# Kernel tuning notes

Hardware: AMD Instinct MI355X
Metric: run time of the kernel (lower is better)

Reference implementation:

```python
import jax, jax.numpy as jnp
import numpy as np

D_MODEL = 1024
NUM_HEADS = 16
D_K = D_MODEL // NUM_HEADS  # 64
THETA = 10000.0


def apply_rope(t, positions):
    # t: [b, h, s, d], positions: [s] int
    d = t.shape[-1]
    inv_freq = 1.0 / (THETA ** (jnp.arange(0, d, 2, dtype=jnp.float32) / d))  # [d/2]
    ang = positions.astype(jnp.float32)[:, None] * inv_freq[None, :]  # [s, d/2]
    cos = jnp.cos(ang)[None, None]  # [1,1,s,d/2]
    sin = jnp.sin(ang)[None, None]
    x1 = t[..., 0::2]
    x2 = t[..., 1::2]
    r1 = x1 * cos - x2 * sin
    r2 = x1 * sin + x2 * cos
    # interleave back: [..., d/2, 2] -> [..., d]
    return jnp.stack([r1, r2], axis=-1).reshape(t.shape)


def setup_inputs() -> dict:
    key = jax.random.key(0)
    ks = jax.random.split(key, 5)
    b, s = 4, 2048
    scale = 1.0 / np.sqrt(D_MODEL)
    return {
        "x": jax.random.normal(ks[0], (b, s, D_MODEL), dtype=jnp.float32),
        "Wq": jax.random.normal(ks[1], (D_MODEL, D_MODEL), dtype=jnp.float32) * scale,
        "Wk": jax.random.normal(ks[2], (D_MODEL, D_MODEL), dtype=jnp.float32) * scale,
        "Wv": jax.random.normal(ks[3], (D_MODEL, D_MODEL), dtype=jnp.float32) * scale,
        "Wo": jax.random.normal(ks[4], (D_MODEL, D_MODEL), dtype=jnp.float32) * scale,
        "token_positions": jnp.arange(s, dtype=jnp.int32),
    }


def reference(x, Wq, Wk, Wv, Wo, token_positions):
    b, s, _ = x.shape
    # nn.Linear with no bias: y = x @ W.T
    def proj(W):
        y = jnp.einsum('bsd,ed->bse', x, W)
        return y.reshape(b, s, NUM_HEADS, D_K).transpose(0, 2, 1, 3)  # [b,h,s,dk]
    Q = apply_rope(proj(Wq), token_positions)
    K = apply_rope(proj(Wk), token_positions)
    V = proj(Wv)
    scores = jnp.einsum('bhqd,bhkd->bhqk', Q, K) / np.sqrt(D_K).astype(np.float32)
    causal = jnp.arange(s)[:, None] >= jnp.arange(s)[None, :]  # [s,s] lower-tri True
    scores = jnp.where(causal[None, None], scores, -jnp.inf)
    probs = jax.nn.softmax(scores, axis=-1)
    out = jnp.einsum('bhqk,bhkd->bhqd', probs, V)  # [b,h,s,dk]
    out = out.transpose(0, 2, 1, 3).reshape(b, s, D_MODEL)
    return jnp.einsum('bsd,ed->bse', out, Wo)
```

## Files before the change

### kernel.cpp

```cpp
#include <hip/hip_runtime.h>
#include <stdint.h>

#define SLEN 2048
#define DMODEL 1024
#define NHEADS 16
#define MTOT 8192

typedef short s16x8 __attribute__((ext_vector_type(8)));
typedef short s16x4 __attribute__((ext_vector_type(4)));
typedef float f32x4 __attribute__((ext_vector_type(4)));
typedef float f32x16 __attribute__((ext_vector_type(16)));
typedef unsigned u32x2 __attribute__((ext_vector_type(2)));
typedef unsigned u32x4 __attribute__((ext_vector_type(4)));

static __device__ __forceinline__ unsigned short f2bf(float f) {
  unsigned u = __builtin_bit_cast(unsigned, f);
  u += 0x7fffu + ((u >> 16) & 1u);
  return (unsigned short)(u >> 16);
}

static __device__ __forceinline__ unsigned cvt_pk_bf16(float lo, float hi) {
  unsigned r;
  asm("v_cvt_pk_bf16_f32 %0, %1, %2" : "=v"(r) : "v"(lo), "v"(hi));
  return r;
}

static __device__ __forceinline__ void gload_lds16(const void* g, void* l) {
  __builtin_amdgcn_global_load_lds((__attribute__((address_space(1))) void*)g,
                                   (__attribute__((address_space(3))) void*)l,
                                   16, 0, 0);
}

#define EXP2R(x) __builtin_amdgcn_exp2f(x)

#define MFMA16(a, b, c) __builtin_amdgcn_mfma_f32_16x16x32_bf16(a, b, c, 0, 0, 0)
#define MFMA32(a, b, c) __builtin_amdgcn_mfma_f32_32x32x16_bf16(a, b, c, 0, 0, 0)
#define SWZ(r) ((((r) & 7) ^ (((r) >> 3) & 7)))

__global__ void __launch_bounds__(256) rope_table(const int* __restrict__ pos,
                                                  float* __restrict__ ctab,
                                                  float* __restrict__ stab) {
  int g = blockIdx.x * 256 + threadIdx.x;
  int s = g >> 5, i = g & 31;
  float p = (float)pos[s];
  float ang = p * exp2f(-(float)i * 0.41524101186092029f);
  ctab[g] = cosf(ang);
  stab[g] = sinf(ang);
}

__global__ void __launch_bounds__(256) cvt_f32_bf16(const float* __restrict__ src,
                                                    unsigned short* __restrict__ dst,
                                                    int n8) {
  int i = blockIdx.x * 256 + threadIdx.x;
  if (i >= n8) return;
  f32x4 a = ((const f32x4*)src)[i * 2];
  f32x4 b = ((const f32x4*)src)[i * 2 + 1];
  s16x8 o;
#pragma unroll
  for (int j = 0; j < 4; ++j) o[j] = (short)f2bf(a[j]);
#pragma unroll
  for (int j = 0; j < 4; ++j) o[4 + j] = (short)f2bf(b[j]);
  ((s16x8*)dst)[i] = o;
}

__global__ void __launch_bounds__(256) cvt_weights(const float* __restrict__ w0,
                                                   const float* __restrict__ w1,
                                                   const float* __restrict__ w2,
                                                   const float* __restrict__ w3,
                                                   unsigned short* __restrict__ d0,
                                                   unsigned short* __restrict__ d1,
                                                   unsigned short* __restrict__ d2,
                                                   unsigned short* __restrict__ d3) {
  int which = blockIdx.y;
  const float* src = which == 0 ? w0 : which == 1 ? w1 : which == 2 ? w2 : w3;
  unsigned short* dst = which == 0 ? d0 : which == 1 ? d1 : which == 2 ? d2 : d3;
  int i = blockIdx.x * 256 + threadIdx.x;
  f32x4 a = ((const f32x4*)src)[i * 2];
  f32x4 b = ((const f32x4*)src)[i * 2 + 1];
  s16x8 o;
#pragma unroll
  for (int j = 0; j < 4; ++j) o[j] = (short)f2bf(a[j]);
#pragma unroll
  for (int j = 0; j < 4; ++j) o[4 + j] = (short)f2bf(b[j]);
  ((s16x8*)dst)[i] = o;
}

template<int MODE>
__global__ void __launch_bounds__(256) gemm_nt(const unsigned short* __restrict__ A,
                                               const unsigned short* __restrict__ B,
                                               void* __restrict__ dstQ,
                                               void* __restrict__ dstK,
                                               void* __restrict__ dstV,
                                               const float* __restrict__ ctab,
                                               const float* __restrict__ stab,
                                               float scale) {
  __shared__ unsigned short ldsA[3][128 * 32];
  __shared__ unsigned short ldsB[3][128 * 32];
  const int tid = threadIdx.x;
  const int lane = tid & 63;
  const int wave = tid >> 6;
  const int wm = wave >> 1, wn = wave & 1;

  int m0, n0;
  if constexpr (MODE == 3) {
    int flat = blockIdx.y * 24 + blockIdx.x;
    int xcd = flat & 7, idx = flat >> 3;
    int g = idx >> 6;
    int local = idx & 63;
    int lm = local >> 3, ln = local & 7;
    m0 = (xcd * 8 + lm) * 128;
    n0 = (g * 8 + ln) * 128;
  } else {
    int flat = blockIdx.y * 8 + blockIdx.x;
    int logical = (flat & 7) * 64 + (flat >> 3);
    m0 = (logical >> 3) * 128;
    n0 = (logical & 7) * 128;
  }
  const int l15 = lane & 15, lhi = lane >> 4;

  f32x4 acc[4][4] = {};

  auto stage = [&](int buf, int kt) {
    const int kbase = kt * 32;
#pragma unroll
    for (int issue = 0; issue < 2; ++issue) {
      int c = issue * 256 + wave * 64 + lane;
      int row = c >> 2, kc = c & 3;
      int kcg = kc ^ ((row >> 1) & 3);
      gload_lds16(A + (size_t)(m0 + row) * 1024 + kbase + kcg * 8,
                  &ldsA[buf][(issue * 256 + wave * 64) * 8]);
      gload_lds16(B + (size_t)(n0 + row) * 1024 + kbase + kcg * 8,
                  &ldsB[buf][(issue * 256 + wave * 64) * 8]);
    }
  };

  stage(0, 0);
  stage(1, 1);
  for (int kt = 0; kt < 32; ++kt) {
    if (kt + 1 < 32) {
      asm volatile("s_waitcnt vmcnt(4)" ::: "memory");
    } else {
      asm volatile("s_waitcnt vmcnt(0)" ::: "memory");
    }
    __builtin_amdgcn_s_barrier();
    __builtin_amdgcn_sched_barrier(0);
    if (kt + 2 < 32) stage((kt + 2) % 3, kt + 2);

    const int buf = kt % 3;
    s16x8 af[4], bf[4];
#pragma unroll
    for (int mi = 0; mi < 4; ++mi) {
      int row = wm * 64 + mi * 16 + l15;
      int kc = lhi ^ ((row >> 1) & 3);
      af[mi] = *(const s16x8*)&ldsA[buf][row * 32 + kc * 8];
    }
#pragma unroll
    for (int ni = 0; ni < 4; ++ni) {
      int row = wn * 64 + ni * 16 + l15;
      int kc = lhi ^ ((row >> 1) & 3);
      bf[ni] = *(const s16x8*)&ldsB[buf][row * 32 + kc * 8];
    }
#pragma unroll
    for (int mi = 0; mi < 4; ++mi)
#pragma unroll
      for (int ni = 0; ni < 4; ++ni)
        acc[mi][ni] = MFMA16(af[mi], bf[ni], acc[mi][ni]);
  }

  if constexpr (MODE == 0) {
    float* dst = (float*)dstQ;
#pragma unroll
    for (int mi = 0; mi < 4; ++mi)
#pragma unroll
      for (int ni = 0; ni < 4; ++ni)
#pragma unroll
        for (int i = 0; i < 4; ++i) {
          int r = m0 + wm * 64 + mi * 16 + lhi * 4 + i;
          int n = n0 + wn * 64 + ni * 16 + l15;
          dst[(size_t)r * 1024 + n] = acc[mi][ni][i];
        }
  } else {
    const int which = n0 >> 10;
    if (which < 2) {
      unsigned short* dst = (unsigned short*)(which == 0 ? dstQ : dstK);
      const float sc = (which == 0) ? scale : 1.0f;
#pragma unroll
      for (int mi = 0; mi < 4; ++mi)
#pragma unroll
        for (int ni = 0; ni < 4; ++ni)
#pragma unroll
          for (int i = 0; i < 4; ++i) {
            int r = m0 + wm * 64 + mi * 16 + lhi * 4 + i;
            int nn = (n0 & 1023) + wn * 64 + ni * 16 + l15;
            float v = acc[mi][ni][i];
            float p = __shfl_xor(v, 1);
            int s = r & (SLEN - 1);
            int d = nn & 63;
            int fi = d >> 1;
            float c = ctab[s * 32 + fi], sn = stab[s * 32 + fi];
            float o = (d & 1) ? (p * sn + v * c) : (v * c - p * sn);
            o *= sc;
            int b = r >> 11, h = nn >> 6;
            dst[((size_t)(b * NHEADS + h) * SLEN + s) * 64 + d] = f2bf(o);
          }
    } else {
      unsigned short* dst = (unsigned short*)dstV;
#pragma unroll
      for (int mi = 0; mi < 4; ++mi)
#pragma unroll
        for (int ni = 0; ni < 4; ++ni) {
          int r0 = m0 + wm * 64 + mi * 16 + lhi * 4;
          int nn = (n0 & 1023) + wn * 64 + ni * 16 + l15;
          int b = r0 >> 11, s0 = r0 & (SLEN - 1);
          int h = nn >> 6, d = nn & 63;
          s16x4 pk;
#pragma unroll
          for (int i = 0; i < 4; ++i) pk[i] = (short)f2bf(acc[mi][ni][i]);
          *(s16x4*)&dst[((size_t)(b * NHEADS + h) * 64 + d) * SLEN + s0] = pk;
        }
    }
  }
}

__global__ void __launch_bounds__(256, 4) flash_attn(const unsigned short* __restrict__ Q,
                                                     const unsigned short* __restrict__ K,
                                                     const unsigned short* __restrict__ Vt,
                                                     unsigned short* __restrict__ Obf) {
  __shared__ unsigned short Kbuf[2][64 * 64];
  __shared__ unsigned short Vbuf[2][64 * 64];

  const int tid = threadIdx.x, lane = tid & 63, w = tid >> 6;
  const int l31 = lane & 31, h = lane >> 5;

  int id = blockIdx.x;
  int xcd = id & 7, idx = id >> 3;
  const int s_ = idx & 3;
  const int bhl = (idx >> 2) & 7;
  const int g_ = idx >> 5;
  const int mul2g = (g_ == 0) ? 0 : (g_ == 1) ? 2 : (g_ == 2) ? 3 : 1;
  const int t = 4 * (s_ ^ g_) + (s_ ^ mul2g);
  const int bh = xcd * 8 + bhl;
  const int b = bh >> 4, hd = bh & 15;

  const unsigned short* Qb = Q + (size_t)bh * SLEN * 64;
  const unsigned short* Kb = K + (size_t)bh * SLEN * 64;
  const unsigned short* Vb = Vt + (size_t)bh * 64 * SLEN;

  const int qbase = t * 128;
  const int nt = 2 * t + 2;
  const int q_abs = qbase + w * 32 + l31;
  const int qminw = qbase + w * 32;

  auto stageKV = [&](int buf, int k0) {
#pragma unroll
    for (int i = 0; i < 2; ++i) {
      int c = i * 256 + tid;
      int row = c >> 3, cg = c & 7;
      int col = ((cg ^ SWZ(row)) * 8);
      gload_lds16(Kb + (size_t)(k0 + row) * 64 + col, &Kbuf[buf][c * 8]);
      gload_lds16(Vb + (size_t)row * SLEN + k0 + col, &Vbuf[buf][c * 8]);
    }
  };

  s16x8 qf[4];
#pragma unroll
  for (int dc = 0; dc < 4; ++dc)
    qf[dc] = *(const s16x8*)&Qb[(size_t)q_abs * 64 + dc * 16 + h * 8];

  f32x16 accT[2] = {};
  float m_run = -3.0e38f, l_run = 0.f;

  stageKV(0, 0);
  for (int kt = 0; kt < nt; ++kt) {
    const int cur = kt & 1;
    const int k0 = kt * 64;
    asm volatile("s_waitcnt vmcnt(0)" ::: "memory");
    __builtin_amdgcn_s_barrier();
    __builtin_amdgcn_sched_barrier(0);
    if (kt + 1 < nt) stageKV(cur ^ 1, (kt + 1) * 64);

    {
      f32x16 sacc[2] = {};
      __builtin_amdgcn_s_setprio(1);
#pragma unroll
      for (int kb = 0; kb < 2; ++kb) {
#pragma unroll
        for (int dc = 0; dc < 4; ++dc) {
          int r = kb * 32 + l31;
          int g = dc * 2 + h;
          s16x8 kf = *(const s16x8*)&Kbuf[cur][r * 64 + ((g ^ SWZ(r)) * 8)];
          sacc[kb] = MFMA32(kf, qf[dc], sacc[kb]);
        }
      }
      __builtin_amdgcn_s_setprio(0);

      if (k0 + 63 > qminw) {
#pragma unroll
        for (int kb = 0; kb < 2; ++kb)
#pragma unroll
          for (int r = 0; r < 16; ++r) {
            int k_abs = k0 + kb * 32 + (r & 3) + 8 * (r >> 2) + 4 * h;
            if (k_abs > q_abs) sacc[kb][r] = -3.0e38f;
          }
      }

      float p0 = fmaxf(sacc[0][0], sacc[1][0]);
      float p1 = fmaxf(sacc[0][1], sacc[1][1]);
      float p2 = fmaxf(sacc[0][2], sacc[1][2]);
      float p3 = fmaxf(sacc[0][3], sacc[1][3]);
#pragma unroll
      for (int r = 4; r < 16; r += 4) {
        p0 = fmaxf(p0, fmaxf(sacc[0][r + 0], sacc[1][r + 0]));
        p1 = fmaxf(p1, fmaxf(sacc[0][r + 1], sacc[1][r + 1]));
        p2 = fmaxf(p2, fmaxf(sacc[0][r + 2], sacc[1][r + 2]));
        p3 = fmaxf(p3, fmaxf(sacc[0][r + 3], sacc[1][r + 3]));
      }
      float mx = fmaxf(fmaxf(p0, p1), fmaxf(p2, p3));
      mx = fmaxf(mx, __shfl_xor(mx, 32));

      if (!__all(mx <= m_run)) {
        float mnew = fmaxf(m_run, mx);
        float facv = EXP2R(m_run - mnew);
        m_run = mnew;
        l_run *= facv;
#pragma unroll
        for (int db = 0; db < 2; ++db)
#pragma unroll
          for (int r = 0; r < 16; ++r) accT[db][r] *= facv;
      }

      float s0 = 0.f, s1 = 0.f, s2 = 0.f, s3 = 0.f;
#pragma unroll
      for (int kb = 0; kb < 2; ++kb)
#pragma unroll
        for (int r = 0; r < 16; r += 4) {
          float e0 = EXP2R(sacc[kb][r + 0] - m_run);
          float e1 = EXP2R(sacc[kb][r + 1] - m_run);
          float e2 = EXP2R(sacc[kb][r + 2] - m_run);
          float e3 = EXP2R(sacc[kb][r + 3] - m_run);
          sacc[kb][r + 0] = e0; sacc[kb][r + 1] = e1;
          sacc[kb][r + 2] = e2; sacc[kb][r + 3] = e3;
          s0 += e0; s1 += e1; s2 += e2; s3 += e3;
        }
      float sum = (s0 + s1) + (s2 + s3);
      sum += __shfl_xor(sum, 32);
      l_run += sum;

      unsigned Hv[8][2];
#pragma unroll
      for (int kb = 0; kb < 2; ++kb)
#pragma unroll
        for (int q4 = 0; q4 < 4; ++q4) {
          Hv[kb * 4 + q4][0] = cvt_pk_bf16(sacc[kb][q4 * 4 + 0], sacc[kb][q4 * 4 + 1]);
          Hv[kb * 4 + q4][1] = cvt_pk_bf16(sacc[kb][q4 * 4 + 2], sacc[kb][q4 * 4 + 3]);
        }

      __builtin_amdgcn_s_setprio(1);
#pragma unroll
      for (int db = 0; db < 2; ++db) {
        int r = db * 32 + l31;
        const char* rowp = (const char*)&Vbuf[cur][r * 64];
#pragma unroll
        for (int kc = 0; kc < 4; ++kc) {
          u32x2 vlo = *(const u32x2*)(rowp + (((2 * kc) ^ SWZ(r)) * 16) + 8 * h);
          u32x2 vhi = *(const u32x2*)(rowp + (((2 * kc + 1) ^ SWZ(r)) * 16) + 8 * h);
          u32x4 vv;
          vv[0] = vlo[0]; vv[1] = vlo[1]; vv[2] = vhi[0]; vv[3] = vhi[1];
          u32x4 pv;
          pv[0] = Hv[2 * kc][0]; pv[1] = Hv[2 * kc][1];
          pv[2] = Hv[2 * kc + 1][0]; pv[3] = Hv[2 * kc + 1][1];
          accT[db] = MFMA32(__builtin_bit_cast(s16x8, vv),
                            __builtin_bit_cast(s16x8, pv), accT[db]);
        }
      }
      __builtin_amdgcn_s_setprio(0);
    }
  }

  float linv = 1.f / l_run;
#pragma unroll
  for (int db = 0; db < 2; ++db)
#pragma unroll
    for (int q4 = 0; q4 < 4; ++q4) {
      u32x2 pk;
      pk[0] = cvt_pk_bf16(accT[db][q4 * 4 + 0] * linv, accT[db][q4 * 4 + 1] * linv);
      pk[1] = cvt_pk_bf16(accT[db][q4 * 4 + 2] * linv, accT[db][q4 * 4 + 3] * linv);
      int d0 = db * 32 + 8 * q4 + 4 * h;
      *(u32x2*)&Obf[((size_t)(b * SLEN + q_abs)) * DMODEL + hd * 64 + d0] = pk;
    }
}

extern "C" void kernel_launch(void* const* d_in, const int* in_sizes, int n_in,
                              void* d_out, int out_size, void* d_ws, size_t ws_size,
                              hipStream_t stream) {
  const float* x  = (const float*)d_in[0];
  const float* Wq = (const float*)d_in[1];
  const float* Wk = (const float*)d_in[2];
  const float* Wv = (const float*)d_in[3];
  const float* Wo = (const float*)d_in[4];
  const int* pos  = (const int*)d_in[5];
  float* out = (float*)d_out;

  char* ws = (char*)d_ws;
  size_t off = 0;
  auto take = [&](size_t bytes) {
    char* p = ws + off;
    off += (bytes + 255) & ~(size_t)255;
    return p;
  };
  unsigned short* xbf  = (unsigned short*)take((size_t)MTOT * DMODEL * 2);
  unsigned short* wqkv = (unsigned short*)take((size_t)3 * DMODEL * DMODEL * 2);
  unsigned short* wobf = (unsigned short*)take((size_t)DMODEL * DMODEL * 2);
  unsigned short* Qs   = (unsigned short*)take((size_t)64 * SLEN * 64 * 2);
  unsigned short* Ks   = (unsigned short*)take((size_t)64 * SLEN * 64 * 2);
  unsigned short* Vt   = (unsigned short*)take((size_t)64 * 64 * SLEN * 2);
  unsigned short* Obf  = (unsigned short*)take((size_t)MTOT * DMODEL * 2);
  float* ctab = (float*)take((size_t)SLEN * 32 * 4);
  float* stab = (float*)take((size_t)SLEN * 32 * 4);

  rope_table<<<256, 256, 0, stream>>>(pos, ctab, stab);
  cvt_f32_bf16<<<4096, 256, 0, stream>>>(x, xbf, MTOT * DMODEL / 8);
  cvt_weights<<<dim3(512, 4), 256, 0, stream>>>(
      Wq, Wk, Wv, Wo,
      wqkv, wqkv + (size_t)DMODEL * DMODEL, wqkv + (size_t)2 * DMODEL * DMODEL, wobf);

  gemm_nt<3><<<dim3(24, 64), 256, 0, stream>>>(xbf, wqkv, Qs, Ks, Vt,
                                               ctab, stab, 0.18033688011112042f);

  flash_attn<<<1024, 256, 0, stream>>>(Qs, Ks, Vt, Obf);

  gemm_nt<0><<<dim3(8, 64), 256, 0, stream>>>(Obf, wobf, out, nullptr, nullptr,
                                              nullptr, nullptr, 1.0f);
}
```

Baseline: 178.2 us.

## Fuse prep kernels and enlarge QKV GEMM tile to 256x128 with 512 threads

Merges the rope-table, x conversion and weight conversion kernels into one prep launch to cut launch overhead. The QKV projection GEMM becomes a dedicated kernel with 256-row M tiles and 8 waves, so each B tile is reused across twice as many rows. Per-block LDS grows and the block count halves (768 blocks), which may lower occupancy. The output projection keeps the old 128x128 path in its own kernel.

```diff
diff --git a/kernel.cpp b/kernel.cpp
--- a/kernel.cpp
+++ b/kernel.cpp
@@ -37,63 +37,172 @@
 #define MFMA32(a, b, c) __builtin_amdgcn_mfma_f32_32x32x16_bf16(a, b, c, 0, 0, 0)
 #define SWZ(r) ((((r) & 7) ^ (((r) >> 3) & 7)))
 
-__global__ void __launch_bounds__(256) rope_table(const int* __restrict__ pos,
-                                                  float* __restrict__ ctab,
-                                                  float* __restrict__ stab) {
-  int g = blockIdx.x * 256 + threadIdx.x;
-  int s = g >> 5, i = g & 31;
-  float p = (float)pos[s];
-  float ang = p * exp2f(-(float)i * 0.41524101186092029f);
-  ctab[g] = cosf(ang);
-  stab[g] = sinf(ang);
-}
-
-__global__ void __launch_bounds__(256) cvt_f32_bf16(const float* __restrict__ src,
-                                                    unsigned short* __restrict__ dst,
-                                                    int n8) {
-  int i = blockIdx.x * 256 + threadIdx.x;
-  if (i >= n8) return;
-  f32x4 a = ((const f32x4*)src)[i * 2];
-  f32x4 b = ((const f32x4*)src)[i * 2 + 1];
-  s16x8 o;
-#pragma unroll
-  for (int j = 0; j < 4; ++j) o[j] = (short)f2bf(a[j]);
-#pragma unroll
-  for (int j = 0; j < 4; ++j) o[4 + j] = (short)f2bf(b[j]);
-  ((s16x8*)dst)[i] = o;
-}
-
-__global__ void __launch_bounds__(256) cvt_weights(const float* __restrict__ w0,
-                                                   const float* __restrict__ w1,
-                                                   const float* __restrict__ w2,
-                                                   const float* __restrict__ w3,
-                                                   unsigned short* __restrict__ d0,
-                                                   unsigned short* __restrict__ d1,
-                                                   unsigned short* __restrict__ d2,
-                                                   unsigned short* __restrict__ d3) {
-  int which = blockIdx.y;
-  const float* src = which == 0 ? w0 : which == 1 ? w1 : which == 2 ? w2 : w3;
-  unsigned short* dst = which == 0 ? d0 : which == 1 ? d1 : which == 2 ? d2 : d3;
-  int i = blockIdx.x * 256 + threadIdx.x;
-  f32x4 a = ((const f32x4*)src)[i * 2];
-  f32x4 b = ((const f32x4*)src)[i * 2 + 1];
-  s16x8 o;
-#pragma unroll
-  for (int j = 0; j < 4; ++j) o[j] = (short)f2bf(a[j]);
-#pragma unroll
-  for (int j = 0; j < 4; ++j) o[4 + j] = (short)f2bf(b[j]);
-  ((s16x8*)dst)[i] = o;
-}
-
-template<int MODE>
-__global__ void __launch_bounds__(256) gemm_nt(const unsigned short* __restrict__ A,
+__global__ void __launch_bounds__(256) prep(const float* __restrict__ x,
+                                            const float* __restrict__ Wq,
+                                            const float* __restrict__ Wk,
+                                            const float* __restrict__ Wv,
+                                            const float* __restrict__ Wo,
+                                            const int* __restrict__ pos,
+                                            unsigned short* __restrict__ xbf,
+                                            unsigned short* __restrict__ wqkv,
+                                            unsigned short* __restrict__ wobf,
+                                            float* __restrict__ ctab,
+                                            float* __restrict__ stab) {
+  int blk = blockIdx.x;
+  if (blk < 4096) {
+    int i = blk * 256 + threadIdx.x;
+    f32x4 a = ((const f32x4*)x)[i * 2];
+    f32x4 b = ((const f32x4*)x)[i * 2 + 1];
+    s16x8 o;
+#pragma unroll
+    for (int j = 0; j < 4; ++j) o[j] = (short)f2bf(a[j]);
+#pragma unroll
+    for (int j = 0; j < 4; ++j) o[4 + j] = (short)f2bf(b[j]);
+    ((s16x8*)xbf)[i] = o;
+  } else if (blk < 6144) {
+    int wsel = (blk - 4096) >> 9;
+    const float* src = wsel == 0 ? Wq : wsel == 1 ? Wk : wsel == 2 ? Wv : Wo;
+    unsigned short* dst = (wsel < 3) ? (wqkv + (size_t)wsel * DMODEL * DMODEL) : wobf;
+    int i = ((blk - 4096) & 511) * 256 + threadIdx.x;
+    f32x4 a = ((const f32x4*)src)[i * 2];
+    f32x4 b = ((const f32x4*)src)[i * 2 + 1];
+    s16x8 o;
+#pragma unroll
+    for (int j = 0; j < 4; ++j) o[j] = (short)f2bf(a[j]);
+#pragma unroll
+    for (int j = 0; j < 4; ++j) o[4 + j] = (short)f2bf(b[j]);
+    ((s16x8*)dst)[i] = o;
+  } else {
+    int g = (blk - 6144) * 256 + threadIdx.x;
+    int s = g >> 5, i = g & 31;
+    float p = (float)pos[s];
+    float ang = p * exp2f(-(float)i * 0.41524101186092029f);
+    ctab[g] = cosf(ang);
+    stab[g] = sinf(ang);
+  }
+}
+
+__global__ void __launch_bounds__(512) gemm_qkv(const unsigned short* __restrict__ A,
+                                                const unsigned short* __restrict__ B,
+                                                unsigned short* __restrict__ dstQ,
+                                                unsigned short* __restrict__ dstK,
+                                                unsigned short* __restrict__ dstV,
+                                                const float* __restrict__ ctab,
+                                                const float* __restrict__ stab,
+                                                float scale) {
+  __shared__ unsigned short ldsA[3][256 * 32];
+  __shared__ unsigned short ldsB[3][128 * 32];
+  const int tid = threadIdx.x;
+  const int lane = tid & 63;
+  const int wave = tid >> 6;
+  const int wm = wave >> 1, wn = wave & 1;
+
+  int flat = blockIdx.y * 24 + blockIdx.x;
+  int xcd = flat & 7, idx = flat >> 3;
+  int g = idx >> 5;
+  int local = idx & 31;
+  int lm = local >> 3, ln = local & 7;
+  const int m0 = (xcd * 4 + lm) * 256;
+  const int n0 = (g * 8 + ln) * 128;
+  const int l15 = lane & 15, lhi = lane >> 4;
+
+  f32x4 acc[4][4] = {};
+
+  auto stage = [&](int buf, int kt) {
+    const int kbase = kt * 32;
+#pragma unroll
+    for (int issue = 0; issue < 2; ++issue) {
+      int c = issue * 512 + wave * 64 + lane;
+      int row = c >> 2, kc = c & 3;
+      int kcg = kc ^ ((row >> 1) & 3);
+      gload_lds16(A + (size_t)(m0 + row) * 1024 + kbase + kcg * 8,
+                  &ldsA[buf][c * 8]);
+    }
+    {
+      int c = wave * 64 + lane;
+      int row = c >> 2, kc = c & 3;
+      int kcg = kc ^ ((row >> 1) & 3);
+      gload_lds16(B + (size_t)(n0 + row) * 1024 + kbase + kcg * 8,
+                  &ldsB[buf][c * 8]);
+    }
+  };
+
+  stage(0, 0);
+  stage(1, 1);
+  for (int kt = 0; kt < 32; ++kt) {
+    if (kt + 1 < 32) {
+      asm volatile("s_waitcnt vmcnt(3)" ::: "memory");
+    } else {
+      asm volatile("s_waitcnt vmcnt(0)" ::: "memory");
+    }
+    __builtin_amdgcn_s_barrier();
+    __builtin_amdgcn_sched_barrier(0);
+    if (kt + 2 < 32) stage((kt + 2) % 3, kt + 2);
+
+    const int buf = kt % 3;
+    s16x8 af[4], bf[4];
+#pragma unroll
+    for (int mi = 0; mi < 4; ++mi) {
+      int row = wm * 64 + mi * 16 + l15;
+      int kc = lhi ^ ((row >> 1) & 3);
+      af[mi] = *(const s16x8*)&ldsA[buf][row * 32 + kc * 8];
+    }
+#pragma unroll
+    for (int ni = 0; ni < 4; ++ni) {
+      int row = wn * 64 + ni * 16 + l15;
+      int kc = lhi ^ ((row >> 1) & 3);
+      bf[ni] = *(const s16x8*)&ldsB[buf][row * 32 + kc * 8];
+    }
+#pragma unroll
+    for (int mi = 0; mi < 4; ++mi)
+#pragma unroll
+      for (int ni = 0; ni < 4; ++ni)
+        acc[mi][ni] = MFMA16(af[mi], bf[ni], acc[mi][ni]);
+  }
+
+  const int which = n0 >> 10;
+  if (which < 2) {
+    unsigned short* dst = (which == 0) ? dstQ : dstK;
+    const float sc = (which == 0) ? scale : 1.0f;
+#pragma unroll
+    for (int mi = 0; mi < 4; ++mi)
+#pragma unroll
+      for (int ni = 0; ni < 4; ++ni)
+#pragma unroll
+        for (int i = 0; i < 4; ++i) {
+          int r = m0 + wm * 64 + mi * 16 + lhi * 4 + i;
+          int nn = (n0 & 1023) + wn * 64 + ni * 16 + l15;
+          float v = acc[mi][ni][i];
+          float p = __shfl_xor(v, 1);
+          int s = r & (SLEN - 1);
+          int d = nn & 63;
+          int fi = d >> 1;
+          float c = ctab[s * 32 + fi], sn = stab[s * 32 + fi];
+          float o = (d & 1) ? (p * sn + v * c) : (v * c - p * sn);
+          o *= sc;
+          int b = r >> 11, h = nn >> 6;
+          dst[((size_t)(b * NHEADS + h) * SLEN + s) * 64 + d] = f2bf(o);
+        }
+  } else {
+#pragma unroll
+    for (int mi = 0; mi < 4; ++mi)
+#pragma unroll
+      for (int ni = 0; ni < 4; ++ni) {
+        int r0 = m0 + wm * 64 + mi * 16 + lhi * 4;
+        int nn = (n0 & 1023) + wn * 64 + ni * 16 + l15;
+        int b = r0 >> 11, s0 = r0 & (SLEN - 1);
+        int h = nn >> 6, d = nn & 63;
+        s16x4 pk;
+#pragma unroll
+        for (int i = 0; i < 4; ++i) pk[i] = (short)f2bf(acc[mi][ni][i]);
+        *(s16x4*)&dstV[((size_t)(b * NHEADS + h) * 64 + d) * SLEN + s0] = pk;
+      }
+  }
+}
+
+__global__ void __launch_bounds__(256) gemm_wo(const unsigned short* __restrict__ A,
                                                const unsigned short* __restrict__ B,
-                                               void* __restrict__ dstQ,
-                                               void* __restrict__ dstK,
-                                               void* __restrict__ dstV,
-                                               const float* __restrict__ ctab,
-                                               const float* __restrict__ stab,
-                                               float scale) {
+                                               float* __restrict__ dst) {
   __shared__ unsigned short ldsA[3][128 * 32];
   __shared__ unsigned short ldsB[3][128 * 32];
   const int tid = threadIdx.x;
@@ -101,21 +210,10 @@
   const int wave = tid >> 6;
   const int wm = wave >> 1, wn = wave & 1;
 
-  int m0, n0;
-  if constexpr (MODE == 3) {
-    int flat = blockIdx.y * 24 + blockIdx.x;
-    int xcd = flat & 7, idx = flat >> 3;
-    int g = idx >> 6;
-    int local = idx & 63;
-    int lm = local >> 3, ln = local & 7;
-    m0 = (xcd * 8 + lm) * 128;
-    n0 = (g * 8 + ln) * 128;
-  } else {
-    int flat = blockIdx.y * 8 + blockIdx.x;
-    int logical = (flat & 7) * 64 + (flat >> 3);
-    m0 = (logical >> 3) * 128;
-    n0 = (logical & 7) * 128;
-  }
+  int flat = blockIdx.y * 8 + blockIdx.x;
+  int logical = (flat & 7) * 64 + (flat >> 3);
+  const int m0 = (logical >> 3) * 128;
+  const int n0 = (logical & 7) * 128;
   const int l15 = lane & 15, lhi = lane >> 4;
 
   f32x4 acc[4][4] = {};
@@ -167,59 +265,16 @@
         acc[mi][ni] = MFMA16(af[mi], bf[ni], acc[mi][ni]);
   }
 
-  if constexpr (MODE == 0) {
-    float* dst = (float*)dstQ;
-#pragma unroll
-    for (int mi = 0; mi < 4; ++mi)
-#pragma unroll
-      for (int ni = 0; ni < 4; ++ni)
-#pragma unroll
-        for (int i = 0; i < 4; ++i) {
-          int r = m0 + wm * 64 + mi * 16 + lhi * 4 + i;
-          int n = n0 + wn * 64 + ni * 16 + l15;
-          dst[(size_t)r * 1024 + n] = acc[mi][ni][i];
-        }
-  } else {
-    const int which = n0 >> 10;
-    if (which < 2) {
-      unsigned short* dst = (unsigned short*)(which == 0 ? dstQ : dstK);
-      const float sc = (which == 0) ? scale : 1.0f;
-#pragma unroll
-      for (int mi = 0; mi < 4; ++mi)
-#pragma unroll
-        for (int ni = 0; ni < 4; ++ni)
-#pragma unroll
-          for (int i = 0; i < 4; ++i) {
-            int r = m0 + wm * 64 + mi * 16 + lhi * 4 + i;
-            int nn = (n0 & 1023) + wn * 64 + ni * 16 + l15;
-            float v = acc[mi][ni][i];
-            float p = __shfl_xor(v, 1);
-            int s = r & (SLEN - 1);
-            int d = nn & 63;
-            int fi = d >> 1;
-            float c = ctab[s * 32 + fi], sn = stab[s * 32 + fi];
-            float o = (d & 1) ? (p * sn + v * c) : (v * c - p * sn);
-            o *= sc;
-            int b = r >> 11, h = nn >> 6;
-            dst[((size_t)(b * NHEADS + h) * SLEN + s) * 64 + d] = f2bf(o);
-          }
-    } else {
-      unsigned short* dst = (unsigned short*)dstV;
-#pragma unroll
-      for (int mi = 0; mi < 4; ++mi)
-#pragma unroll
-        for (int ni = 0; ni < 4; ++ni) {
-          int r0 = m0 + wm * 64 + mi * 16 + lhi * 4;
-          int nn = (n0 & 1023) + wn * 64 + ni * 16 + l15;
-          int b = r0 >> 11, s0 = r0 & (SLEN - 1);
-          int h = nn >> 6, d = nn & 63;
-          s16x4 pk;
-#pragma unroll
-          for (int i = 0; i < 4; ++i) pk[i] = (short)f2bf(acc[mi][ni][i]);
-          *(s16x4*)&dst[((size_t)(b * NHEADS + h) * 64 + d) * SLEN + s0] = pk;
-        }
-    }
-  }
+#pragma unroll
+  for (int mi = 0; mi < 4; ++mi)
+#pragma unroll
+    for (int ni = 0; ni < 4; ++ni)
+#pragma unroll
+      for (int i = 0; i < 4; ++i) {
+        int r = m0 + wm * 64 + mi * 16 + lhi * 4 + i;
+        int n = n0 + wn * 64 + ni * 16 + l15;
+        dst[(size_t)r * 1024 + n] = acc[mi][ni][i];
+      }
 }
 
 __global__ void __launch_bounds__(256, 4) flash_attn(const unsigned short* __restrict__ Q,
@@ -418,17 +473,13 @@
   float* ctab = (float*)take((size_t)SLEN * 32 * 4);
   float* stab = (float*)take((size_t)SLEN * 32 * 4);
 
-  rope_table<<<256, 256, 0, stream>>>(pos, ctab, stab);
-  cvt_f32_bf16<<<4096, 256, 0, stream>>>(x, xbf, MTOT * DMODEL / 8);
-  cvt_weights<<<dim3(512, 4), 256, 0, stream>>>(
-      Wq, Wk, Wv, Wo,
-      wqkv, wqkv + (size_t)DMODEL * DMODEL, wqkv + (size_t)2 * DMODEL * DMODEL, wobf);
-
-  gemm_nt<3><<<dim3(24, 64), 256, 0, stream>>>(xbf, wqkv, Qs, Ks, Vt,
-                                               ctab, stab, 0.18033688011112042f);
+  prep<<<6400, 256, 0, stream>>>(x, Wq, Wk, Wv, Wo, pos,
+                                 xbf, wqkv, wobf, ctab, stab);
+
+  gemm_qkv<<<dim3(24, 32), 512, 0, stream>>>(xbf, wqkv, Qs, Ks, Vt,
+                                             ctab, stab, 0.18033688011112042f);
 
   flash_attn<<<1024, 256, 0, stream>>>(Qs, Ks, Vt, Obf);
 
-  gemm_nt<0><<<dim3(8, 64), 256, 0, stream>>>(Obf, wobf, out, nullptr, nullptr,
-                                              nullptr, nullptr, 1.0f);
-}
+  gemm_wo<<<dim3(8, 64), 256, 0, stream>>>(Obf, wobf, out);
+}
```

Measured after the change: 172.4 us. 3.2% less time.
